# Kernel optimization log

Hardware: AMD Instinct MI355X
Metric: run time of the kernel (lower is better)

Reference implementation:

```python
import jax, jax.numpy as jnp
import numpy as np

B, HH, WW = 4, 112, 112
DIM, NH, WS, SHIFT = 384, 12, 7, 3
N = WS * WS
HD = DIM // NH
SCALE = HD ** -0.5
HID = DIM * 4
NW = (HH // WS) * (WW // WS)


def _ln(x, w, b):
    m = x.mean(-1, keepdims=True)
    v = ((x - m) ** 2).mean(-1, keepdims=True)
    return (x - m) / jnp.sqrt(v + 1e-5) * w + b


def _win_part(x):  # (B,H,W,C) -> (B*nW, N, C)
    x = x.reshape(B, HH // WS, WS, WW // WS, WS, DIM).transpose(0, 1, 3, 2, 4, 5)
    return x.reshape(-1, N, DIM)


def _win_rev(w):  # (B*nW, N, C) -> (B,H,W,C)
    x = w.reshape(B, HH // WS, WW // WS, WS, WS, DIM).transpose(0, 1, 3, 2, 4, 5)
    return x.reshape(B, HH, WW, DIM)


def _rel_index():
    c = np.arange(WS)
    coords = np.stack(np.meshgrid(c, c, indexing='ij')).reshape(2, -1)
    rel = (coords[:, :, None] - coords[:, None, :]).transpose(1, 2, 0).copy()
    rel[:, :, 0] += WS - 1
    rel[:, :, 1] += WS - 1
    rel[:, :, 0] *= 2 * WS - 1
    return rel.sum(-1)  # (N, N)


def _attn_mask():
    img = np.zeros((HH, WW))
    cnt = 0
    for hs in (slice(0, -WS), slice(-WS, -SHIFT), slice(-SHIFT, None)):
        for ws_ in (slice(0, -WS), slice(-WS, -SHIFT), slice(-SHIFT, None)):
            img[hs, ws_] = cnt
            cnt += 1
    mw = img.reshape(HH // WS, WS, WW // WS, WS).transpose(0, 2, 1, 3).reshape(-1, N)
    am = mw[:, None, :] - mw[:, :, None]
    return np.where(am != 0, -100.0, 0.0).astype(np.float32)  # (nW, N, N)


def setup_inputs():
    key = jax.random.key(0)
    ks = iter(jax.random.split(key, 32))
    rn = lambda shape, s=0.02: jax.random.normal(next(ks), shape, jnp.float32) * s
    return {
        'branch_1': jax.random.normal(next(ks), (B, HH * WW, DIM), jnp.float32),
        'branch_2': jax.random.normal(next(ks), (B, HH * WW, DIM), jnp.float32),
        'mask_matrix': jnp.asarray(_attn_mask()),
        'rpi': jnp.asarray(_rel_index(), jnp.int32),
        'n1w1': jnp.ones((DIM,)), 'n1b1': jnp.zeros((DIM,)),
        'n1w2': jnp.ones((DIM,)), 'n1b2': jnp.zeros((DIM,)),
        'qw1': rn((3 * DIM, DIM)), 'qb1': jnp.zeros((3 * DIM,)),
        'qw2': rn((3 * DIM, DIM)), 'qb2': jnp.zeros((3 * DIM,)),
        'rpb1': rn(((2 * WS - 1) ** 2, NH)), 'rpb2': rn(((2 * WS - 1) ** 2, NH)),
        'pw1': rn((DIM, DIM)), 'pb1': jnp.zeros((DIM,)),
        'pw2': rn((DIM, DIM)), 'pb2': jnp.zeros((DIM,)),
        'n2w1': jnp.ones((DIM,)), 'n2b1': jnp.zeros((DIM,)),
        'n2w2': jnp.ones((DIM,)), 'n2b2': jnp.zeros((DIM,)),
        'm1fc1w': rn((HID, DIM)), 'm1fc1b': jnp.zeros((HID,)),
        'm1fc2w': rn((DIM, HID)), 'm1fc2b': jnp.zeros((DIM,)),
        'm2fc1w': rn((HID, DIM)), 'm2fc1b': jnp.zeros((HID,)),
        'm2fc2w': rn((DIM, HID)), 'm2fc2b': jnp.zeros((DIM,)),
    }


def _cross_attn(x1, x2, mask, rpi, qw1, qb1, qw2, qb2, rpb1, rpb2, pw1, pb1, pw2, pb2):
    Bw = x1.shape[0]

    def qkv(x, w, b):
        t = (x @ w.T + b).reshape(Bw, N, 3, NH, HD).transpose(2, 0, 3, 1, 4)
        return t[0], t[1], t[2]

    q1, k1, v1 = qkv(x1, qw1, qb1)
    q2, k2, v2 = qkv(x2, qw2, qb2)
    a1 = (q2 * SCALE) @ jnp.swapaxes(k1, -2, -1)  # (Bw, NH, N, N)
    a2 = (q1 * SCALE) @ jnp.swapaxes(k2, -2, -1)
    b1 = rpb1[rpi].transpose(2, 0, 1)  # (NH, N, N)
    b2 = rpb2[rpi].transpose(2, 0, 1)
    a1 = a1 + b1[None]
    a2 = a2 + b2[None]
    nW = mask.shape[0]
    a1 = (a1.reshape(Bw // nW, nW, NH, N, N) + mask[None, :, None]).reshape(Bw, NH, N, N)
    a2 = (a2.reshape(Bw // nW, nW, NH, N, N) + mask[None, :, None]).reshape(Bw, NH, N, N)
    a1 = jax.nn.softmax(a1, axis=-1)
    a2 = jax.nn.softmax(a2, axis=-1)
    o1 = (a1 @ v1).transpose(0, 2, 1, 3).reshape(Bw, N, DIM) @ pw1.T + pb1
    o2 = (a2 @ v2).transpose(0, 2, 1, 3).reshape(Bw, N, DIM) @ pw2.T + pb2
    del o2
    return o1, o1  # faithful to original: it returns [branch_1, branch_1]


def _mlp(x, w1, b1, w2, b2):
    return jax.nn.gelu(x @ w1.T + b1, approximate=False) @ w2.T + b2


def reference(branch_1, branch_2, mask_matrix, rpi, n1w1, n1b1, n1w2, n1b2,
              qw1, qb1, qw2, qb2, rpb1, rpb2, pw1, pb1, pw2, pb2,
              n2w1, n2b1, n2w2, n2b2,
              m1fc1w, m1fc1b, m1fc2w, m1fc2b, m2fc1w, m2fc1b, m2fc2w, m2fc2b):
    s1, s2 = branch_1, branch_2
    x1 = _ln(branch_1, n1w1, n1b1).reshape(B, HH, WW, DIM)
    x2 = _ln(branch_2, n1w2, n1b2).reshape(B, HH, WW, DIM)
    # cyclic shift (shift_size > 0; H,W divisible by window_size so no padding)
    x1 = jnp.roll(x1, (-SHIFT, -SHIFT), (1, 2))
    x2 = jnp.roll(x2, (-SHIFT, -SHIFT), (1, 2))
    w1, w2 = _win_part(x1), _win_part(x2)
    o1, o2 = _cross_attn(w1, w2, mask_matrix, rpi, qw1, qb1, qw2, qb2,
                         rpb1, rpb2, pw1, pb1, pw2, pb2)
    y1 = jnp.roll(_win_rev(o1), (SHIFT, SHIFT), (1, 2)).reshape(B, HH * WW, DIM)
    y2 = jnp.roll(_win_rev(o2), (SHIFT, SHIFT), (1, 2)).reshape(B, HH * WW, DIM)
    b1 = s1 + y1
    b2 = s2 + y2
    out1 = b1 + _mlp(_ln(b1, n2w1, n2b1), m1fc1w, m1fc1b, m1fc2w, m1fc2b)
    out2 = b2 + _mlp(_ln(b2, n2w2, n2b2), m2fc1w, m2fc1b, m2fc2w, m2fc2b)
    return out1, out2
```

## Files before the change

### kernel.cpp

```cpp
#include <hip/hip_runtime.h>
#include <math.h>

#define DEV __device__ __forceinline__

typedef __attribute__((ext_vector_type(8))) unsigned short u16x8;
typedef __attribute__((ext_vector_type(8))) __bf16 bf16x8;
typedef __attribute__((ext_vector_type(4))) float f32x4;

static constexpr int TOK = 50176;
static constexpr int DIMC = 384;
static constexpr float QSCALE = 0.17677669529663687f;

DEV unsigned short f2bf(float f) {
  union { float f; unsigned u; } v; v.f = f;
  unsigned r = v.u + 0x7fffu + ((v.u >> 16) & 1u);
  return (unsigned short)(r >> 16);
}

DEV f32x4 mfma16(bf16x8 a, bf16x8 b, f32x4 c) {
  return __builtin_amdgcn_mfma_f32_16x16x32_bf16(a, b, c, 0, 0, 0);
}

DEV void gload_lds16(const void* g, void* lds) {
  __builtin_amdgcn_global_load_lds(
      (const __attribute__((address_space(1))) void*)g,
      (__attribute__((address_space(3))) void*)lds, 16, 0, 0);
}

__global__ __launch_bounds__(256) void w2bf_kern(const float* __restrict__ in,
                                                 unsigned short* __restrict__ out, int n) {
  int i = blockIdx.x * 256 + threadIdx.x;
  if (i < n) out[i] = f2bf(in[i]);
}

template<bool WINDOW>
__global__ __launch_bounds__(256) void ln_kern(const float* __restrict__ in,
                                               const float* __restrict__ gw,
                                               const float* __restrict__ gb,
                                               unsigned short* __restrict__ out) {
  const int row = blockIdx.x * 4 + (threadIdx.x >> 6);
  const int l = threadIdx.x & 63;
  int src = row;
  if (WINDOW) {
    const int wq = row / 49, nn = row - wq * 49;
    const int bb = wq >> 8, wi = wq & 255;
    int hh = (wi >> 4) * 7 + nn / 7 + 3;        if (hh >= 112) hh -= 112;
    int cc = (wi & 15) * 7 + (nn - (nn / 7) * 7) + 3; if (cc >= 112) cc -= 112;
    src = bb * 12544 + hh * 112 + cc;
  }
  const float* x = in + (size_t)src * DIMC;
  float v[6]; float s = 0.f, s2 = 0.f;
#pragma unroll
  for (int j = 0; j < 6; ++j) { float t = x[l + 64 * j]; v[j] = t; s += t; s2 += t * t; }
#pragma unroll
  for (int d = 1; d < 64; d <<= 1) { s += __shfl_xor(s, d); s2 += __shfl_xor(s2, d); }
  const float mean = s * (1.f / 384.f);
  const float var = s2 * (1.f / 384.f) - mean * mean;
  const float rs = rsqrtf(var + 1e-5f);
#pragma unroll
  for (int j = 0; j < 6; ++j) {
    int c = l + 64 * j;
    out[(size_t)row * DIMC + c] = f2bf((v[j] - mean) * rs * gw[c] + gb[c]);
  }
}

enum { E_BF16 = 0, E_BF16_SCALE = 1, E_SCATTER = 2, E_GELU = 3, E_RESOUT = 4 };

template<int EPI>
__global__ __launch_bounds__(256) void gemm_bt(
    const unsigned short* __restrict__ A, const unsigned short* __restrict__ W,
    const float* __restrict__ bias, int K, int N, int nbx,
    unsigned short* __restrict__ outb,
    float* __restrict__ outf1, float* __restrict__ outf2,
    const float* __restrict__ res1, const float* __restrict__ res2) {
  __shared__ __align__(16) unsigned short sA[3][128 * 32];
  __shared__ __align__(16) unsigned short sB[3][128 * 32];
  const int t = threadIdx.x;
  const int wv = t >> 6, l = t & 63;
  const int wm = (wv >> 1) * 64, wn = (wv & 1) * 64;

  const int total = gridDim.x;
  const int q = total >> 3, rr8 = total & 7;
  const int xcd = blockIdx.x & 7, lid = blockIdx.x >> 3;
  const int wgid = (xcd < rr8 ? xcd * (q + 1) : rr8 * (q + 1) + (xcd - rr8) * q) + lid;
  const int n0 = (wgid % nbx) * 128, m0 = (wgid / nbx) * 128;

  const int srow = t >> 2;
  const int scol = ((t & 3) ^ ((t >> 3) & 3)) * 8;

  f32x4 acc[4][4];
  const f32x4 fzero = {0.f, 0.f, 0.f, 0.f};
#pragma unroll
  for (int i = 0; i < 4; ++i)
#pragma unroll
    for (int j = 0; j < 4; ++j) acc[i][j] = fzero;

  const unsigned short* gA = A + (size_t)(m0 + srow) * K + scol;
  const unsigned short* gB = W + (size_t)(n0 + srow) * K + scol;
  const int ldsW = wv * 512;

  const int g = l >> 4, lr = l & 15;
  const int swz = ((lr >> 1) & 3) << 4;

  const int ntt = K >> 5;
#pragma unroll
  for (int p = 0; p < 2; ++p) {
#pragma unroll
    for (int it = 0; it < 2; ++it) {
      gload_lds16(gA + (size_t)(it * 64) * K + p * 32, &sA[p][it * 2048 + ldsW]);
      gload_lds16(gB + (size_t)(it * 64) * K + p * 32, &sB[p][it * 2048 + ldsW]);
    }
  }
  for (int tt = 0; tt < ntt; ++tt) {
    if (tt + 1 < ntt) {
      asm volatile("s_waitcnt vmcnt(4)" ::: "memory");
    } else {
      asm volatile("s_waitcnt vmcnt(0)" ::: "memory");
    }
    __builtin_amdgcn_s_barrier();
    asm volatile("" ::: "memory");
    if (tt + 2 < ntt) {
      const int kt = (tt + 2) << 5;
      const int b2 = (tt + 2) % 3;
#pragma unroll
      for (int it = 0; it < 2; ++it) {
        gload_lds16(gA + (size_t)(it * 64) * K + kt, &sA[b2][it * 2048 + ldsW]);
        gload_lds16(gB + (size_t)(it * 64) * K + kt, &sB[b2][it * 2048 + ldsW]);
      }
    }
    const int cb = tt % 3;
    const char* bA = (const char*)&sA[cb][0];
    const char* bB = (const char*)&sB[cb][0];
    bf16x8 af[4], bff[4];
#pragma unroll
    for (int mt = 0; mt < 4; ++mt)
      af[mt] = *(const bf16x8*)(bA + (wm + mt * 16 + lr) * 64 + ((g * 16) ^ swz));
#pragma unroll
    for (int nt2 = 0; nt2 < 4; ++nt2)
      bff[nt2] = *(const bf16x8*)(bB + (wn + nt2 * 16 + lr) * 64 + ((g * 16) ^ swz));
    __builtin_amdgcn_s_setprio(1);
#pragma unroll
    for (int mt = 0; mt < 4; ++mt)
#pragma unroll
      for (int nt2 = 0; nt2 < 4; ++nt2)
        acc[mt][nt2] = mfma16(af[mt], bff[nt2], acc[mt][nt2]);
    __builtin_amdgcn_s_setprio(0);
    asm volatile("" ::: "memory");
  }

  const int col = lr;
#pragma unroll
  for (int mt = 0; mt < 4; ++mt) {
#pragma unroll
    for (int r = 0; r < 4; ++r) {
      const int m = m0 + wm + mt * 16 + g * 4 + r;
      size_t obase = 0;
      if constexpr (EPI == E_SCATTER) {
        int wq = m / 49, nn = m - wq * 49;
        int bb = wq >> 8, wi = wq & 255;
        int hh = (wi >> 4) * 7 + nn / 7 + 3;        if (hh >= 112) hh -= 112;
        int cc = (wi & 15) * 7 + (nn - (nn / 7) * 7) + 3; if (cc >= 112) cc -= 112;
        obase = ((size_t)bb * 12544 + hh * 112 + cc) * 384;
      }
#pragma unroll
      for (int nt2 = 0; nt2 < 4; ++nt2) {
        const int j = n0 + wn + nt2 * 16 + col;
        float v = acc[mt][nt2][r] + bias[j];
        if constexpr (EPI == E_BF16) {
          outb[(size_t)m * N + j] = f2bf(v);
        } else if constexpr (EPI == E_BF16_SCALE) {
          outb[(size_t)m * N + j] = f2bf(v * QSCALE);
        } else if constexpr (EPI == E_GELU) {
          float z = v * (1.5957691216057308f + 0.0713548162726009f * v * v);
          float gg = v / (1.f + __expf(-z));
          outb[(size_t)m * N + j] = f2bf(gg);
        } else if constexpr (EPI == E_SCATTER) {
          outf1[obase + j] = res1[obase + j] + v;
          outf2[obase + j] = res2[obase + j] + v;
        } else {
          outf1[(size_t)m * N + j] = v + res1[(size_t)m * N + j];
        }
      }
    }
  }
}

__global__ __launch_bounds__(256) void attn_kern(
    const unsigned short* __restrict__ q2,
    const unsigned short* __restrict__ kv1,
    const int* __restrict__ rpi,
    const float* __restrict__ mask,
    const float* __restrict__ rpb,
    unsigned short* __restrict__ o) {
  const int w = blockIdx.x, h = blockIdx.y;
  __shared__ __align__(16) unsigned short sQ[64 * 32];
  __shared__ __align__(16) unsigned short sK[64 * 32];
  __shared__ __align__(16) unsigned short sVT[32 * 64];
  __shared__ __align__(16) unsigned short sP[64 * 64];
  const int t = threadIdx.x, wv = t >> 6, l = t & 63;
  const int r = t >> 2, c = (t & 3) * 8;
  const u16x8 z8 = {0, 0, 0, 0, 0, 0, 0, 0};
  if (r < 49) {
    *(u16x8*)&sQ[r * 32 + c] = *(const u16x8*)&q2[((size_t)w * 49 + r) * 384 + h * 32 + c];
    *(u16x8*)&sK[r * 32 + c] = *(const u16x8*)&kv1[((size_t)w * 49 + r) * 768 + h * 32 + c];
    u16x8 vv = *(const u16x8*)&kv1[((size_t)w * 49 + r) * 768 + 384 + h * 32 + c];
#pragma unroll
    for (int e = 0; e < 8; ++e) sVT[(c + e) * 64 + r] = vv[e];
  } else {
    *(u16x8*)&sQ[r * 32 + c] = z8;
    *(u16x8*)&sK[r * 32 + c] = z8;
#pragma unroll
    for (int e = 0; e < 8; ++e) sVT[(c + e) * 64 + r] = 0;
  }
  __syncthreads();

  const int g = l >> 4, col = l & 15;
  const f32x4 fzero = {0.f, 0.f, 0.f, 0.f};
  bf16x8 aq = *(const bf16x8*)&sQ[(wv * 16 + col) * 32 + g * 8];
  f32x4 s[4];
#pragma unroll
  for (int nt = 0; nt < 4; ++nt) {
    bf16x8 bk = *(const bf16x8*)&sK[(nt * 16 + col) * 32 + g * 8];
    s[nt] = mfma16(aq, bk, fzero);
  }

  const int wi = w & 255;
  float p[4][4];
#pragma unroll
  for (int rr = 0; rr < 4; ++rr) {
    const int i = wv * 16 + g * 4 + rr;
    float mx = -1e30f;
#pragma unroll
    for (int nt = 0; nt < 4; ++nt) {
      const int j = nt * 16 + col;
      float val = -1e9f;
      if (i < 49 && j < 49)
        val = s[nt][rr] + rpb[rpi[i * 49 + j] * 12 + h] + mask[((size_t)wi * 49 + i) * 49 + j];
      p[nt][rr] = val;
      mx = fmaxf(mx, val);
    }
#pragma unroll
    for (int d = 1; d < 16; d <<= 1) mx = fmaxf(mx, __shfl_xor(mx, d));
    float sm = 0.f;
#pragma unroll
    for (int nt = 0; nt < 4; ++nt) {
      const int j = nt * 16 + col;
      float e = (j < 49) ? __expf(p[nt][rr] - mx) : 0.f;
      p[nt][rr] = e; sm += e;
    }
#pragma unroll
    for (int d = 1; d < 16; d <<= 1) sm += __shfl_xor(sm, d);
    const float inv = 1.f / sm;
#pragma unroll
    for (int nt = 0; nt < 4; ++nt) p[nt][rr] *= inv;
  }
#pragma unroll
  for (int rr = 0; rr < 4; ++rr) {
    const int i = wv * 16 + g * 4 + rr;
#pragma unroll
    for (int nt = 0; nt < 4; ++nt) sP[i * 64 + nt * 16 + col] = f2bf(p[nt][rr]);
  }
  __syncthreads();

  f32x4 oa[2] = {fzero, fzero};
#pragma unroll
  for (int ks = 0; ks < 2; ++ks) {
    bf16x8 ap = *(const bf16x8*)&sP[(wv * 16 + col) * 64 + ks * 32 + g * 8];
#pragma unroll
    for (int n2 = 0; n2 < 2; ++n2) {
      bf16x8 bv = *(const bf16x8*)&sVT[(n2 * 16 + col) * 64 + ks * 32 + g * 8];
      oa[n2] = mfma16(ap, bv, oa[n2]);
    }
  }
#pragma unroll
  for (int rr = 0; rr < 4; ++rr) {
    const int i = wv * 16 + g * 4 + rr;
    if (i < 49) {
#pragma unroll
      for (int n2 = 0; n2 < 2; ++n2)
        o[((size_t)w * 49 + i) * 384 + h * 32 + n2 * 16 + col] = f2bf(oa[n2][rr]);
    }
  }
}

extern "C" void kernel_launch(void* const* d_in, const int* in_sizes, int n_in,
                              void* d_out, int out_size, void* d_ws, size_t ws_size,
                              hipStream_t stream) {
  (void)in_sizes; (void)n_in; (void)out_size; (void)ws_size;
  const float* s1   = (const float*)d_in[0];
  const float* s2   = (const float*)d_in[1];
  const float* mask = (const float*)d_in[2];
  const int*   rpi  = (const int*)d_in[3];
  const float* n1w1 = (const float*)d_in[4],  *n1b1 = (const float*)d_in[5];
  const float* n1w2 = (const float*)d_in[6],  *n1b2 = (const float*)d_in[7];
  const float* qw1  = (const float*)d_in[8],  *qb1  = (const float*)d_in[9];
  const float* qw2  = (const float*)d_in[10], *qb2  = (const float*)d_in[11];
  const float* rpb1 = (const float*)d_in[12];
  const float* pw1  = (const float*)d_in[14], *pb1  = (const float*)d_in[15];
  const float* n2w1 = (const float*)d_in[18], *n2b1 = (const float*)d_in[19];
  const float* n2w2 = (const float*)d_in[20], *n2b2 = (const float*)d_in[21];
  const float* m1fc1w = (const float*)d_in[22], *m1fc1b = (const float*)d_in[23];
  const float* m1fc2w = (const float*)d_in[24], *m1fc2b = (const float*)d_in[25];
  const float* m2fc1w = (const float*)d_in[26], *m2fc1b = (const float*)d_in[27];
  const float* m2fc2w = (const float*)d_in[28], *m2fc2b = (const float*)d_in[29];

  char* ws = (char*)d_ws;
  const size_t S1 = (size_t)TOK * DIMC * 2;
  unsigned short* x1w  = (unsigned short*)(ws);
  unsigned short* x2w  = (unsigned short*)(ws + S1);
  unsigned short* kv1  = (unsigned short*)(ws + 2 * S1);
  unsigned short* q2b  = (unsigned short*)(ws + 4 * S1);
  unsigned short* obuf = x1w;
  unsigned short* hbuf = x2w;
  unsigned short* xm   = x1w;
  char* wp = ws + 5 * S1;
  unsigned short* wq1b = (unsigned short*)(wp);
  unsigned short* wq2b = (unsigned short*)(wp + 589824);
  unsigned short* wp1b = (unsigned short*)(wp + 884736);
  unsigned short* wf11 = (unsigned short*)(wp + 1179648);
  unsigned short* wf12 = (unsigned short*)(wp + 2359296);
  unsigned short* wf21 = (unsigned short*)(wp + 3538944);
  unsigned short* wf22 = (unsigned short*)(wp + 4718592);

  float* outf = (float*)d_out;
  float* b1 = outf;
  float* b2 = outf + (size_t)19267584;

  w2bf_kern<<<(294912 + 255) / 256, 256, 0, stream>>>(qw1 + 384 * 384, wq1b, 294912);
  w2bf_kern<<<(147456 + 255) / 256, 256, 0, stream>>>(qw2, wq2b, 147456);
  w2bf_kern<<<(147456 + 255) / 256, 256, 0, stream>>>(pw1, wp1b, 147456);
  w2bf_kern<<<(589824 + 255) / 256, 256, 0, stream>>>(m1fc1w, wf11, 589824);
  w2bf_kern<<<(589824 + 255) / 256, 256, 0, stream>>>(m1fc2w, wf12, 589824);
  w2bf_kern<<<(589824 + 255) / 256, 256, 0, stream>>>(m2fc1w, wf21, 589824);
  w2bf_kern<<<(589824 + 255) / 256, 256, 0, stream>>>(m2fc2w, wf22, 589824);

  ln_kern<true><<<TOK / 4, 256, 0, stream>>>(s1, n1w1, n1b1, x1w);
  ln_kern<true><<<TOK / 4, 256, 0, stream>>>(s2, n1w2, n1b2, x2w);

  gemm_bt<E_BF16><<<6 * 392, 256, 0, stream>>>(x1w, wq1b, qb1 + 384, 384, 768, 6,
                                               kv1, nullptr, nullptr, nullptr, nullptr);
  gemm_bt<E_BF16_SCALE><<<3 * 392, 256, 0, stream>>>(x2w, wq2b, qb2, 384, 384, 3,
                                                     q2b, nullptr, nullptr, nullptr, nullptr);
  attn_kern<<<dim3(1024, 12), 256, 0, stream>>>(q2b, kv1, rpi, mask, rpb1, obuf);

  gemm_bt<E_SCATTER><<<3 * 392, 256, 0, stream>>>(obuf, wp1b, pb1, 384, 384, 3,
                                                  nullptr, b1, b2, s1, s2);
  ln_kern<false><<<TOK / 4, 256, 0, stream>>>(b1, n2w1, n2b1, xm);
  gemm_bt<E_GELU><<<12 * 392, 256, 0, stream>>>(xm, wf11, m1fc1b, 384, 1536, 12,
                                                hbuf, nullptr, nullptr, nullptr, nullptr);
  gemm_bt<E_RESOUT><<<3 * 392, 256, 0, stream>>>(hbuf, wf12, m1fc2b, 1536, 384, 3,
                                                 nullptr, b1, nullptr, b1, nullptr);
  ln_kern<false><<<TOK / 4, 256, 0, stream>>>(b2, n2w2, n2b2, xm);
  gemm_bt<E_GELU><<<12 * 392, 256, 0, stream>>>(xm, wf21, m2fc1b, 384, 1536, 12,
                                                hbuf, nullptr, nullptr, nullptr, nullptr);
  gemm_bt<E_RESOUT><<<3 * 392, 256, 0, stream>>>(hbuf, wf22, m2fc2b, 1536, 384, 3,
                                                 nullptr, b2, nullptr, b2, nullptr);
}
```

Measured before the change: 855.7 us.

## Use persistent 256x128 GEMM tiles with 512-thread blocks and grid-stride loop

The GEMM kernel now runs as a persistent grid of 512 blocks of 512 threads. Each block loops over 256x128 output tiles, and eight waves share one B tile, so B traffic per output drops. The XCD-aware tile remapping becomes a fixed formula, and the s_setprio hints are removed. In exchange, the larger LDS footprint (72KB) may limit occupancy, and tile-count tails can leave some CUs idle.

```diff
diff --git a/kernel.cpp b/kernel.cpp
--- a/kernel.cpp
+++ b/kernel.cpp
@@ -67,118 +67,112 @@
 enum { E_BF16 = 0, E_BF16_SCALE = 1, E_SCATTER = 2, E_GELU = 3, E_RESOUT = 4 };
 
 template<int EPI>
-__global__ __launch_bounds__(256) void gemm_bt(
+__global__ __launch_bounds__(512, 4) void gemm_bt(
     const unsigned short* __restrict__ A, const unsigned short* __restrict__ W,
-    const float* __restrict__ bias, int K, int N, int nbx,
+    const float* __restrict__ bias, int K, int N, int nbx, int ntiles,
     unsigned short* __restrict__ outb,
     float* __restrict__ outf1, float* __restrict__ outf2,
     const float* __restrict__ res1, const float* __restrict__ res2) {
-  __shared__ __align__(16) unsigned short sA[3][128 * 32];
+  __shared__ __align__(16) unsigned short sA[3][256 * 32];
   __shared__ __align__(16) unsigned short sB[3][128 * 32];
   const int t = threadIdx.x;
   const int wv = t >> 6, l = t & 63;
   const int wm = (wv >> 1) * 64, wn = (wv & 1) * 64;
 
-  const int total = gridDim.x;
-  const int q = total >> 3, rr8 = total & 7;
-  const int xcd = blockIdx.x & 7, lid = blockIdx.x >> 3;
-  const int wgid = (xcd < rr8 ? xcd * (q + 1) : rr8 * (q + 1) + (xcd - rr8) * q) + lid;
-  const int n0 = (wgid % nbx) * 128, m0 = (wgid / nbx) * 128;
+  const int wgid0 = (blockIdx.x & 7) * 64 + (blockIdx.x >> 3);
 
   const int srow = t >> 2;
-  const int scol = ((t & 3) ^ ((t >> 3) & 3)) * 8;
-
-  f32x4 acc[4][4];
-  const f32x4 fzero = {0.f, 0.f, 0.f, 0.f};
-#pragma unroll
-  for (int i = 0; i < 4; ++i)
-#pragma unroll
-    for (int j = 0; j < 4; ++j) acc[i][j] = fzero;
-
-  const unsigned short* gA = A + (size_t)(m0 + srow) * K + scol;
-  const unsigned short* gB = W + (size_t)(n0 + srow) * K + scol;
+  const int scol = ((t & 3) ^ ((srow >> 1) & 3)) * 8;
   const int ldsW = wv * 512;
 
   const int g = l >> 4, lr = l & 15;
   const int swz = ((lr >> 1) & 3) << 4;
-
+  const f32x4 fzero = {0.f, 0.f, 0.f, 0.f};
   const int ntt = K >> 5;
-#pragma unroll
-  for (int p = 0; p < 2; ++p) {
-#pragma unroll
-    for (int it = 0; it < 2; ++it) {
-      gload_lds16(gA + (size_t)(it * 64) * K + p * 32, &sA[p][it * 2048 + ldsW]);
-      gload_lds16(gB + (size_t)(it * 64) * K + p * 32, &sB[p][it * 2048 + ldsW]);
-    }
-  }
-  for (int tt = 0; tt < ntt; ++tt) {
-    if (tt + 1 < ntt) {
-      asm volatile("s_waitcnt vmcnt(4)" ::: "memory");
-    } else {
-      asm volatile("s_waitcnt vmcnt(0)" ::: "memory");
-    }
-    __builtin_amdgcn_s_barrier();
-    asm volatile("" ::: "memory");
-    if (tt + 2 < ntt) {
-      const int kt = (tt + 2) << 5;
-      const int b2 = (tt + 2) % 3;
-#pragma unroll
-      for (int it = 0; it < 2; ++it) {
-        gload_lds16(gA + (size_t)(it * 64) * K + kt, &sA[b2][it * 2048 + ldsW]);
-        gload_lds16(gB + (size_t)(it * 64) * K + kt, &sB[b2][it * 2048 + ldsW]);
+
+  for (int T = wgid0; T < ntiles; T += 512) {
+    const int n0 = (T % nbx) * 128, m0 = (T / nbx) * 256;
+
+    f32x4 acc[4][4];
+#pragma unroll
+    for (int i = 0; i < 4; ++i)
+#pragma unroll
+      for (int j = 0; j < 4; ++j) acc[i][j] = fzero;
+
+    const unsigned short* pA = A + (size_t)(m0 + srow) * K + scol;
+    const unsigned short* pB = W + (size_t)(n0 + srow) * K + scol;
+
+#pragma unroll
+    for (int p = 0; p < 2; ++p) {
+      gload_lds16(pA + p * 32, &sA[p][ldsW]);
+      gload_lds16(pA + (size_t)128 * K + p * 32, &sA[p][4096 + ldsW]);
+      gload_lds16(pB + p * 32, &sB[p][ldsW]);
+    }
+    for (int tt = 0; tt < ntt; ++tt) {
+      if (tt + 1 < ntt) {
+        asm volatile("s_waitcnt vmcnt(3)" ::: "memory");
+      } else {
+        asm volatile("s_waitcnt vmcnt(0)" ::: "memory");
       }
-    }
-    const int cb = tt % 3;
-    const char* bA = (const char*)&sA[cb][0];
-    const char* bB = (const char*)&sB[cb][0];
-    bf16x8 af[4], bff[4];
-#pragma unroll
-    for (int mt = 0; mt < 4; ++mt)
-      af[mt] = *(const bf16x8*)(bA + (wm + mt * 16 + lr) * 64 + ((g * 16) ^ swz));
-#pragma unroll
-    for (int nt2 = 0; nt2 < 4; ++nt2)
-      bff[nt2] = *(const bf16x8*)(bB + (wn + nt2 * 16 + lr) * 64 + ((g * 16) ^ swz));
-    __builtin_amdgcn_s_setprio(1);
-#pragma unroll
-    for (int mt = 0; mt < 4; ++mt)
+      __builtin_amdgcn_s_barrier();
+      asm volatile("" ::: "memory");
+      if (tt + 2 < ntt) {
+        const int kt = (tt + 2) << 5;
+        const int b2 = (tt + 2) % 3;
+        gload_lds16(pA + kt, &sA[b2][ldsW]);
+        gload_lds16(pA + (size_t)128 * K + kt, &sA[b2][4096 + ldsW]);
+        gload_lds16(pB + kt, &sB[b2][ldsW]);
+      }
+      const int cb = tt % 3;
+      const char* bA = (const char*)&sA[cb][0];
+      const char* bB = (const char*)&sB[cb][0];
+      bf16x8 af[4], bff[4];
+#pragma unroll
+      for (int mt = 0; mt < 4; ++mt)
+        af[mt] = *(const bf16x8*)(bA + (wm + mt * 16 + lr) * 64 + ((g * 16) ^ swz));
 #pragma unroll
       for (int nt2 = 0; nt2 < 4; ++nt2)
-        acc[mt][nt2] = mfma16(af[mt], bff[nt2], acc[mt][nt2]);
-    __builtin_amdgcn_s_setprio(0);
-    asm volatile("" ::: "memory");
-  }
-
-  const int col = lr;
-#pragma unroll
-  for (int mt = 0; mt < 4; ++mt) {
-#pragma unroll
-    for (int r = 0; r < 4; ++r) {
-      const int m = m0 + wm + mt * 16 + g * 4 + r;
-      size_t obase = 0;
-      if constexpr (EPI == E_SCATTER) {
-        int wq = m / 49, nn = m - wq * 49;
-        int bb = wq >> 8, wi = wq & 255;
-        int hh = (wi >> 4) * 7 + nn / 7 + 3;        if (hh >= 112) hh -= 112;
-        int cc = (wi & 15) * 7 + (nn - (nn / 7) * 7) + 3; if (cc >= 112) cc -= 112;
-        obase = ((size_t)bb * 12544 + hh * 112 + cc) * 384;
-      }
-#pragma unroll
-      for (int nt2 = 0; nt2 < 4; ++nt2) {
-        const int j = n0 + wn + nt2 * 16 + col;
-        float v = acc[mt][nt2][r] + bias[j];
-        if constexpr (EPI == E_BF16) {
-          outb[(size_t)m * N + j] = f2bf(v);
-        } else if constexpr (EPI == E_BF16_SCALE) {
-          outb[(size_t)m * N + j] = f2bf(v * QSCALE);
-        } else if constexpr (EPI == E_GELU) {
-          float z = v * (1.5957691216057308f + 0.0713548162726009f * v * v);
-          float gg = v / (1.f + __expf(-z));
-          outb[(size_t)m * N + j] = f2bf(gg);
-        } else if constexpr (EPI == E_SCATTER) {
-          outf1[obase + j] = res1[obase + j] + v;
-          outf2[obase + j] = res2[obase + j] + v;
-        } else {
-          outf1[(size_t)m * N + j] = v + res1[(size_t)m * N + j];
+        bff[nt2] = *(const bf16x8*)(bB + (wn + nt2 * 16 + lr) * 64 + ((g * 16) ^ swz));
+#pragma unroll
+      for (int mt = 0; mt < 4; ++mt)
+#pragma unroll
+        for (int nt2 = 0; nt2 < 4; ++nt2)
+          acc[mt][nt2] = mfma16(af[mt], bff[nt2], acc[mt][nt2]);
+      asm volatile("" ::: "memory");
+    }
+
+    const int col = lr;
+#pragma unroll
+    for (int mt = 0; mt < 4; ++mt) {
+#pragma unroll
+      for (int r = 0; r < 4; ++r) {
+        const int m = m0 + wm + mt * 16 + g * 4 + r;
+        size_t obase = 0;
+        if constexpr (EPI == E_SCATTER) {
+          int wq = m / 49, nn = m - wq * 49;
+          int bb = wq >> 8, wi = wq & 255;
+          int hh = (wi >> 4) * 7 + nn / 7 + 3;        if (hh >= 112) hh -= 112;
+          int cc = (wi & 15) * 7 + (nn - (nn / 7) * 7) + 3; if (cc >= 112) cc -= 112;
+          obase = ((size_t)bb * 12544 + hh * 112 + cc) * 384;
+        }
+#pragma unroll
+        for (int nt2 = 0; nt2 < 4; ++nt2) {
+          const int j = n0 + wn + nt2 * 16 + col;
+          float v = acc[mt][nt2][r] + bias[j];
+          if constexpr (EPI == E_BF16) {
+            outb[(size_t)m * N + j] = f2bf(v);
+          } else if constexpr (EPI == E_BF16_SCALE) {
+            outb[(size_t)m * N + j] = f2bf(v * QSCALE);
+          } else if constexpr (EPI == E_GELU) {
+            float z = v * (1.5957691216057308f + 0.0713548162726009f * v * v);
+            float gg = v / (1.f + __expf(-z));
+            outb[(size_t)m * N + j] = f2bf(gg);
+          } else if constexpr (EPI == E_SCATTER) {
+            outf1[obase + j] = res1[obase + j] + v;
+            outf2[obase + j] = res2[obase + j] + v;
+          } else {
+            outf1[(size_t)m * N + j] = v + res1[(size_t)m * N + j];
+          }
         }
       }
     }
@@ -337,22 +331,22 @@
   ln_kern<true><<<TOK / 4, 256, 0, stream>>>(s1, n1w1, n1b1, x1w);
   ln_kern<true><<<TOK / 4, 256, 0, stream>>>(s2, n1w2, n1b2, x2w);
 
-  gemm_bt<E_BF16><<<6 * 392, 256, 0, stream>>>(x1w, wq1b, qb1 + 384, 384, 768, 6,
-                                               kv1, nullptr, nullptr, nullptr, nullptr);
-  gemm_bt<E_BF16_SCALE><<<3 * 392, 256, 0, stream>>>(x2w, wq2b, qb2, 384, 384, 3,
-                                                     q2b, nullptr, nullptr, nullptr, nullptr);
+  gemm_bt<E_BF16><<<512, 512, 0, stream>>>(x1w, wq1b, qb1 + 384, 384, 768, 6, 1176,
+                                           kv1, nullptr, nullptr, nullptr, nullptr);
+  gemm_bt<E_BF16_SCALE><<<512, 512, 0, stream>>>(x2w, wq2b, qb2, 384, 384, 3, 588,
+                                                 q2b, nullptr, nullptr, nullptr, nullptr);
   attn_kern<<<dim3(1024, 12), 256, 0, stream>>>(q2b, kv1, rpi, mask, rpb1, obuf);
 
-  gemm_bt<E_SCATTER><<<3 * 392, 256, 0, stream>>>(obuf, wp1b, pb1, 384, 384, 3,
-                                                  nullptr, b1, b2, s1, s2);
+  gemm_bt<E_SCATTER><<<512, 512, 0, stream>>>(obuf, wp1b, pb1, 384, 384, 3, 588,
+                                              nullptr, b1, b2, s1, s2);
   ln_kern<false><<<TOK / 4, 256, 0, stream>>>(b1, n2w1, n2b1, xm);
-  gemm_bt<E_GELU><<<12 * 392, 256, 0, stream>>>(xm, wf11, m1fc1b, 384, 1536, 12,
-                                                hbuf, nullptr, nullptr, nullptr, nullptr);
-  gemm_bt<E_RESOUT><<<3 * 392, 256, 0, stream>>>(hbuf, wf12, m1fc2b, 1536, 384, 3,
-                                                 nullptr, b1, nullptr, b1, nullptr);
+  gemm_bt<E_GELU><<<512, 512, 0, stream>>>(xm, wf11, m1fc1b, 384, 1536, 12, 2352,
+                                           hbuf, nullptr, nullptr, nullptr, nullptr);
+  gemm_bt<E_RESOUT><<<512, 512, 0, stream>>>(hbuf, wf12, m1fc2b, 1536, 384, 3, 588,
+                                             nullptr, b1, nullptr, b1, nullptr);
   ln_kern<false><<<TOK / 4, 256, 0, stream>>>(b2, n2w2, n2b2, xm);
-  gemm_bt<E_GELU><<<12 * 392, 256, 0, stream>>>(xm, wf21, m2fc1b, 384, 1536, 12,
-                                                hbuf, nullptr, nullptr, nullptr, nullptr);
-  gemm_bt<E_RESOUT><<<3 * 392, 256, 0, stream>>>(hbuf, wf22, m2fc2b, 1536, 384, 3,
-                                                 nullptr, b2, nullptr, b2, nullptr);
-}
+  gemm_bt<E_GELU><<<512, 512, 0, stream>>>(xm, wf21, m2fc1b, 384, 1536, 12, 2352,
+                                           hbuf, nullptr, nullptr, nullptr, nullptr);
+  gemm_bt<E_RESOUT><<<512, 512, 0, stream>>>(hbuf, wf22, m2fc2b, 1536, 384, 3, 588,
+                                             nullptr, b2, nullptr, b2, nullptr);
+}
```

After: 1.029 ms. +20.2%, slower.
